# Kernel optimization log

Hardware: AMD Instinct MI355X
Metric: run time of the kernel (lower is better)

Reference implementation:

```python
import jax, jax.numpy as jnp
import numpy as np

D_MODEL = 1024

def setup_inputs() -> dict:
    key = jax.random.key(0)
    ks = jax.random.split(key, 5)
    s = 1.0 / np.sqrt(D_MODEL)  # torch Linear default init scale-ish
    x = jax.random.normal(ks[0], (4, 2048, D_MODEL), dtype=jnp.float32)
    Wq = jax.random.normal(ks[1], (D_MODEL, D_MODEL), dtype=jnp.float32) * s
    Wk = jax.random.normal(ks[2], (D_MODEL, D_MODEL), dtype=jnp.float32) * s
    Wv = jax.random.normal(ks[3], (D_MODEL, D_MODEL), dtype=jnp.float32) * s
    Wo = jax.random.normal(ks[4], (D_MODEL, D_MODEL), dtype=jnp.float32) * s
    z = jnp.zeros((D_MODEL,), dtype=jnp.float32)
    return {"x": x, "Wq": Wq, "bq": z, "Wk": Wk, "bk": z, "Wv": Wv, "bv": z, "Wo": Wo, "bo": z}

def reference(x, Wq, bq, Wk, bk, Wv, bv, Wo, bo):
    # x: (B, S, D). Single-head causal attention, dropout in eval mode (identity).
    B, S, D = x.shape
    Q = jnp.einsum('bsd,ed->bse', x, Wq) + bq
    K = jnp.einsum('bsd,ed->bse', x, Wk) + bk
    V = jnp.einsum('bsd,ed->bse', x, Wv) + bv
    scores = jnp.einsum('bqd,bkd->bqk', Q, K) / jnp.sqrt(jnp.float32(D))
    causal = jnp.tril(jnp.ones((S, S), dtype=bool))  # (S, S)
    scores = jnp.where(causal, scores, -jnp.inf)
    weights = jax.nn.softmax(scores, axis=-1)
    attended = jnp.einsum('bqk,bkd->bqd', weights, V)
    out = jnp.einsum('bsd,ed->bse', attended, Wo) + bo
    return out
```

## Files before the change

kernel.cpp:

```cpp
#include <hip/hip_runtime.h>
#include <cstdint>
#include <cstddef>


#define D_MODEL 1024
#define SEQ     2048
#define BATCH   4

typedef unsigned short u16;
typedef __bf16 bf16_t;
typedef bf16_t bf16x8 __attribute__((ext_vector_type(8)));
typedef float  f32x4  __attribute__((ext_vector_type(4)));
typedef u16    u16x4  __attribute__((ext_vector_type(4)));

__device__ __forceinline__ u16 f2bf(float x) {
  union { float f; uint32_t u; } v; v.f = x;
  uint32_t r = v.u + 0x7fffu + ((v.u >> 16) & 1u);
  return (u16)(r >> 16);
}

__device__ __forceinline__ void gload_lds16(const u16* g, u16* l) {
  __builtin_amdgcn_global_load_lds((__attribute__((address_space(1))) void*)g,
                                   (__attribute__((address_space(3))) void*)l,
                                   16, 0, 0);
}

template <bool ROWSUM>
__device__ __forceinline__ void gemm_core(const u16* __restrict__ Ablk,
                                          const u16* __restrict__ Bblk,
                                          int lda, int ldb, int ksteps64,
                                          u16* As, u16* Bs,
                                          f32x4 acc[4][4], f32x4* rs) {
  const int tid  = threadIdx.x;
  const int wave = tid >> 6, lane = tid & 63;
  const int wr = (wave >> 1) * 64, wc = (wave & 1) * 64;
  const int frow = lane & 15, kq = lane >> 4;
  int sm[4], sk[4];
#pragma unroll
  for (int t = 0; t < 4; ++t) {
    const int ch = t * 256 + tid;
    sm[t] = ch >> 3;
    sk[t] = ((ch & 7) ^ (sm[t] & 7)) * 8;
  }
  int aoff[4], boff[4];
#pragma unroll
  for (int i = 0; i < 4; ++i) {
    const int ra = wr + i * 16 + frow;
    aoff[i] = ra * 64 + ((kq ^ (ra & 7)) * 8);
    const int rb = wc + i * 16 + frow;
    boff[i] = rb * 64 + ((kq ^ (rb & 7)) * 8);
  }
  bf16x8 ones;
  if (ROWSUM) {
#pragma unroll
    for (int r = 0; r < 8; ++r) ((u16*)&ones)[r] = 0x3F80;
  }

  for (int kt = 0; kt < ksteps64; ++kt) {
    __syncthreads();
    const int kb = kt * 64;
#pragma unroll
    for (int t = 0; t < 4; ++t)
      gload_lds16(Ablk + sm[t] * lda + kb + sk[t], As + (t * 256 + tid) * 8);
#pragma unroll
    for (int t = 0; t < 4; ++t)
      gload_lds16(Bblk + sm[t] * ldb + kb + sk[t], Bs + (t * 256 + tid) * 8);
    asm volatile("s_waitcnt vmcnt(0)" ::: "memory");
    __syncthreads();

#pragma unroll
    for (int kh = 0; kh < 2; ++kh) {
      const int xo = kh * 32;
      bf16x8 af[4], bf[4];
#pragma unroll
      for (int i = 0; i < 4; ++i) af[i] = *(const bf16x8*)(As + (aoff[i] ^ xo));
#pragma unroll
      for (int j = 0; j < 4; ++j) bf[j] = *(const bf16x8*)(Bs + (boff[j] ^ xo));
#pragma unroll
      for (int i = 0; i < 4; ++i)
#pragma unroll
        for (int j = 0; j < 4; ++j)
          acc[i][j] = __builtin_amdgcn_mfma_f32_16x16x32_bf16(af[i], bf[j], acc[i][j], 0, 0, 0);
      if (ROWSUM) {
#pragma unroll
        for (int i = 0; i < 4; ++i)
          rs[i] = __builtin_amdgcn_mfma_f32_16x16x32_bf16(af[i], ones, rs[i], 0, 0, 0);
      }
    }
  }
}

__global__ __launch_bounds__(256) void cvt_kernel(const float4* __restrict__ x,
                                                  const float4* __restrict__ wq,
                                                  const float4* __restrict__ wk,
                                                  const float4* __restrict__ wv,
                                                  const float4* __restrict__ wo,
                                                  u16* __restrict__ dst) {
  const int i = blockIdx.x * 256 + threadIdx.x;
  float4 v;
  if (i < 2097152) {
    v = x[i];
  } else {
    const int j = i - 2097152;
    const int w = j >> 18;
    const float4* s = (w == 0) ? wq : (w == 1) ? wk : (w == 2) ? wv : wo;
    v = s[j & 262143];
  }
  u16x4 o = {f2bf(v.x), f2bf(v.y), f2bf(v.z), f2bf(v.w)};
  *(u16x4*)(dst + (size_t)i * 4) = o;
}

__global__ void transposeW_kernel(const u16* __restrict__ src, u16* __restrict__ dst) {
  __shared__ u16 tile[32][33];
  const int r0 = blockIdx.x * 32, c0 = blockIdx.y * 32;
  const int tx = threadIdx.x, ty = threadIdx.y;
#pragma unroll
  for (int r = 0; r < 4; ++r)
    tile[ty + r * 8][tx] = src[(size_t)(r0 + ty + r * 8) * D_MODEL + c0 + tx];
  __syncthreads();
#pragma unroll
  for (int r = 0; r < 4; ++r)
    dst[(size_t)(c0 + ty + r * 8) * D_MODEL + r0 + tx] = tile[tx][ty + r * 8];
}

__global__ __launch_bounds__(256) void stageA_kernel(
    const u16* __restrict__ xb,
    const u16* __restrict__ WqB, const u16* __restrict__ WkB,
    const u16* __restrict__ WoB, const u16* __restrict__ WvT,
    const float* __restrict__ Wo32, const float* __restrict__ bv,
    const float* __restrict__ bq, const float* __restrict__ bk,
    u16* __restrict__ Qb, u16* __restrict__ Kb,
    u16* __restrict__ Wp, float* __restrict__ bp) {
  __shared__ __align__(16) u16 As[128 * 64];
  __shared__ __align__(16) u16 Bs[128 * 64];
  const int blk = blockIdx.x;
  const int lane = threadIdx.x & 63, wave = threadIdx.x >> 6;
  const int wr = (wave >> 1) * 64, wc = (wave & 1) * 64;
  const int cl = lane & 15, rl = (lane >> 4) * 4;

  if (blk < 64) {
    const int f0 = (blk >> 3) * 128, e0 = (blk & 7) * 128;
    f32x4 acc[4][4] = {};
    gemm_core<false>(WoB + (size_t)f0 * D_MODEL, WvT + (size_t)e0 * D_MODEL,
                     D_MODEL, D_MODEL, 16, As, Bs, acc, nullptr);
#pragma unroll
    for (int j = 0; j < 4; ++j) {
      const int col = e0 + wc + j * 16 + cl;
#pragma unroll
      for (int i = 0; i < 4; ++i)
#pragma unroll
        for (int r = 0; r < 4; ++r) {
          const int row = f0 + wr + i * 16 + rl + r;
          Wp[(size_t)row * D_MODEL + col] = f2bf(acc[i][j][r]);
        }
    }
  } else if (blk < 80) {
    const int f = (blk - 64) * 64 + (threadIdx.x >> 2);
    const int dq = threadIdx.x & 3;
    const float* row = Wo32 + (size_t)f * D_MODEL + dq * 256;
    const float* bvq = bv + dq * 256;
    float s = 0.f;
#pragma unroll 8
    for (int i = 0; i < 256; ++i) s += row[i] * bvq[i];
    s += __shfl_xor(s, 1);
    s += __shfl_xor(s, 2);
    if (dq == 0) bp[f] = s;
  } else {
    const int v = blk - 80;
    const int c = v & 7, s = v >> 3;
    const int row0 = (c * 8 + (s >> 4)) * 128;
    const int cz = s & 15;
    const int z = cz >> 3;
    const int col0 = (cz & 7) * 128;
    const u16*   W    = z ? WkB : WqB;
    const float* bias = z ? bk : bq;
    u16*         out  = z ? Kb : Qb;
    f32x4 acc[4][4] = {};
    gemm_core<false>(xb + (size_t)row0 * D_MODEL, W + (size_t)col0 * D_MODEL,
                     D_MODEL, D_MODEL, 16, As, Bs, acc, nullptr);
#pragma unroll
    for (int j = 0; j < 4; ++j) {
      const int col = col0 + wc + j * 16 + cl;
      const float bb = bias[col];
#pragma unroll
      for (int i = 0; i < 4; ++i)
#pragma unroll
        for (int r = 0; r < 4; ++r) {
          const int row = row0 + wr + i * 16 + rl + r;
          out[(size_t)row * D_MODEL + col] = f2bf(acc[i][j][r] + bb);
        }
    }
  }
}

__global__ __launch_bounds__(256) void stageB_kernel(
    const u16* __restrict__ xb, const u16* __restrict__ Wp,
    const float* __restrict__ bp,
    const u16* __restrict__ Qb, const u16* __restrict__ Kb,
    u16* __restrict__ Vt, u16* __restrict__ Eb) {
  __shared__ __align__(16) u16 As[128 * 64];
  __shared__ __align__(16) u16 Bs[128 * 64];
  const int blk = blockIdx.x;
  const int lane = threadIdx.x & 63, wave = threadIdx.x >> 6;
  const int wr = (wave >> 1) * 64, wc = (wave & 1) * 64;
  const int cl = lane & 15, rl = (lane >> 4) * 4;

  if (blk < 544) {
    const int c = blk & 7, s = blk >> 3;
    int b, qi, ji;
    if (s < 48) {
      static const int sq_tab[6] = {1, 2, 2, 3, 3, 3};
      static const int sj_tab[6] = {0, 0, 1, 0, 1, 2};
      const int fi = c * 3 + (s >> 4);
      const int off = s & 15;
      b = fi / 6;
      const int fs = fi % 6;
      qi = sq_tab[fs] * 4 + (off >> 2);
      ji = sj_tab[fs] * 4 + (off & 3);
    } else {
      static const int di_tab[10] = {0, 1, 1, 2, 2, 2, 3, 3, 3, 3};
      static const int dj_tab[10] = {0, 0, 1, 0, 1, 2, 0, 1, 2, 3};
      const int k = (s - 48) / 10;
      const int off = (s - 48) % 10;
      const int di = c * 2 + k;
      b = di >> 2;
      const int dk = di & 3;
      qi = dk * 4 + di_tab[off];
      ji = dk * 4 + dj_tab[off];
    }
    const u16* A  = Qb + (size_t)(b * SEQ + qi * 128) * D_MODEL;
    const u16* Bt = Kb + (size_t)(b * SEQ + ji * 128) * D_MODEL;
    f32x4 acc[4][4] = {};
    gemm_core<false>(A, Bt, D_MODEL, D_MODEL, 16, As, Bs, acc, nullptr);
    u16* out = Eb + (size_t)b * SEQ * SEQ;
#pragma unroll
    for (int i = 0; i < 4; ++i)
#pragma unroll
      for (int r = 0; r < 4; ++r) {
        const int q = qi * 128 + wr + i * 16 + rl + r;
#pragma unroll
        for (int j = 0; j < 4; ++j) {
          const int jj = ji * 128 + wc + j * 16 + cl;
          out[(size_t)q * SEQ + jj] =
              (jj <= q) ? f2bf(__expf(acc[i][j][r] * 0.03125f)) : (u16)0;
        }
      }
  } else {
    const int v = blk - 544;
    const int c = v & 7, s = v >> 3;
    const int row0 = (c * 8 + (s >> 3)) * 128;
    const int col0 = (s & 7) * 128;
    f32x4 acc[4][4] = {};
    gemm_core<false>(xb + (size_t)row0 * D_MODEL, Wp + (size_t)col0 * D_MODEL,
                     D_MODEL, D_MODEL, 16, As, Bs, acc, nullptr);
    const int b = row0 >> 11;
    u16* vt = Vt + (size_t)b * D_MODEL * SEQ;
#pragma unroll
    for (int j = 0; j < 4; ++j) {
      const int col = col0 + wc + j * 16 + cl;
      const float bb = bp[col];
#pragma unroll
      for (int i = 0; i < 4; ++i) {
        const int s0 = (row0 & 2047) + wr + i * 16 + rl;
        u16x4 o = {f2bf(acc[i][j][0] + bb), f2bf(acc[i][j][1] + bb),
                   f2bf(acc[i][j][2] + bb), f2bf(acc[i][j][3] + bb)};
        *(u16x4*)(vt + (size_t)col * SEQ + s0) = o;
      }
    }
  }
}

__global__ __launch_bounds__(256) void pv_kernel(const u16* __restrict__ Eb,
                                                 const u16* __restrict__ Vt,
                                                 const float* __restrict__ bo,
                                                 float* __restrict__ Out) {
  __shared__ __align__(16) u16 As[128 * 64];
  __shared__ __align__(16) u16 Bs[128 * 64];
  const int u = blockIdx.x;
  const int c = u & 7, s = u >> 3;
  const int b  = c >> 1;
  const int dt = (c & 1) * 4 + (s >> 4);
  const int qt = 15 - (s & 15);
  const u16* A  = Eb + (size_t)b * SEQ * SEQ + (size_t)(qt * 128) * SEQ;
  const u16* Bt = Vt + (size_t)b * D_MODEL * SEQ + (size_t)(dt * 128) * SEQ;
  f32x4 acc[4][4] = {};
  f32x4 rs[4] = {};
  gemm_core<true>(A, Bt, SEQ, SEQ, (qt + 1) * 2, As, Bs, acc, rs);
  const int lane = threadIdx.x & 63, wave = threadIdx.x >> 6;
  const int wr = (wave >> 1) * 64, wc = (wave & 1) * 64;
  const int cl = lane & 15, rl = (lane >> 4) * 4;
#pragma unroll
  for (int i = 0; i < 4; ++i)
#pragma unroll
    for (int r = 0; r < 4; ++r) {
      const float invl = 1.0f / rs[i][r];
      const int row = b * SEQ + qt * 128 + wr + i * 16 + rl + r;
#pragma unroll
      for (int j = 0; j < 4; ++j) {
        const int col = dt * 128 + wc + j * 16 + cl;
        Out[(size_t)row * D_MODEL + col] = acc[i][j][r] * invl + bo[col];
      }
    }
}

extern "C" void kernel_launch(void* const* d_in, const int* in_sizes, int n_in,
                              void* d_out, int out_size, void* d_ws, size_t ws_size,
                              hipStream_t stream) {
  const float* x  = (const float*)d_in[0];
  const float* Wq = (const float*)d_in[1];
  const float* bq = (const float*)d_in[2];
  const float* Wk = (const float*)d_in[3];
  const float* bk = (const float*)d_in[4];
  const float* Wv = (const float*)d_in[5];
  const float* bv = (const float*)d_in[6];
  const float* Wo = (const float*)d_in[7];
  const float* bo = (const float*)d_in[8];
  float* out = (float*)d_out;
  char* ws = (char*)d_ws;

  u16*   xb  = (u16*)(ws);
  u16*   Wb  = (u16*)(ws + (16u << 20));
  u16*   Qb  = (u16*)(ws + (24u << 20));
  u16*   Kb  = (u16*)(ws + (40u << 20));
  u16*   Vt  = (u16*)(ws + (56u << 20));
  u16*   Eb  = (u16*)(ws + (72u << 20));
  u16*   WvT = (u16*)(ws + (104u << 20));
  u16*   Wp  = (u16*)(ws + (106u << 20));
  float* bp  = (float*)(ws + (108u << 20));

  cvt_kernel<<<12288, 256, 0, stream>>>((const float4*)x, (const float4*)Wq,
                                        (const float4*)Wk, (const float4*)Wv,
                                        (const float4*)Wo, xb);
  transposeW_kernel<<<dim3(32, 32), dim3(32, 8), 0, stream>>>(Wb + (2u << 20), WvT);
  stageA_kernel<<<1104, 256, 0, stream>>>(xb, Wb, Wb + (1u << 20), Wb + (3u << 20),
                                          WvT, Wo, bv, bq, bk, Qb, Kb, Wp, bp);
  stageB_kernel<<<1056, 256, 0, stream>>>(xb, Wp, bp, Qb, Kb, Vt, Eb);
  pv_kernel<<<512, 256, 0, stream>>>(Eb, Vt, bo, out);
}
```

Measured before the change: 268.2 us.

## Double-buffer GEMM core with 32-wide K tiles and prefetch overlap

Replaces the single-buffered 64-wide K-step loop with a double-buffered 32-wide K loop. The next tile's global-to-LDS loads are issued before computing on the current buffer, and a partial vmcnt wait lets the loads overlap the MFMAs. LDS use per block stays the same, and the XOR swizzle is re-derived for 4 chunks per row. The risk is twice as many iterations with two barriers each, plus a redundant final prefetch of the last tile.

```diff
diff --git a/kernel.cpp b/kernel.cpp
--- a/kernel.cpp
+++ b/kernel.cpp
@@ -28,27 +28,23 @@
 template <bool ROWSUM>
 __device__ __forceinline__ void gemm_core(const u16* __restrict__ Ablk,
                                           const u16* __restrict__ Bblk,
-                                          int lda, int ldb, int ksteps64,
+                                          int lda, int ldb, int ksteps32,
                                           u16* As, u16* Bs,
                                           f32x4 acc[4][4], f32x4* rs) {
   const int tid  = threadIdx.x;
   const int wave = tid >> 6, lane = tid & 63;
   const int wr = (wave >> 1) * 64, wc = (wave & 1) * 64;
-  const int frow = lane & 15, kq = lane >> 4;
-  int sm[4], sk[4];
-#pragma unroll
-  for (int t = 0; t < 4; ++t) {
-    const int ch = t * 256 + tid;
-    sm[t] = ch >> 3;
-    sk[t] = ((ch & 7) ^ (sm[t] & 7)) * 8;
-  }
+  const int frow = lane & 15, kc = lane >> 4;
+  const int ch0 = tid, ch1 = 256 + tid;
+  const int m0 = ch0 >> 2, k80 = (((ch0 & 3) ^ ((m0 >> 1) & 3))) * 8;
+  const int m1 = ch1 >> 2, k81 = (((ch1 & 3) ^ ((m1 >> 1) & 3))) * 8;
   int aoff[4], boff[4];
 #pragma unroll
   for (int i = 0; i < 4; ++i) {
     const int ra = wr + i * 16 + frow;
-    aoff[i] = ra * 64 + ((kq ^ (ra & 7)) * 8);
+    aoff[i] = (ra * 4 + (kc ^ ((ra >> 1) & 3))) * 8;
     const int rb = wc + i * 16 + frow;
-    boff[i] = rb * 64 + ((kq ^ (rb & 7)) * 8);
+    boff[i] = (rb * 4 + (kc ^ ((rb >> 1) & 3))) * 8;
   }
   bf16x8 ones;
   if (ROWSUM) {
@@ -56,37 +52,38 @@
     for (int r = 0; r < 8; ++r) ((u16*)&ones)[r] = 0x3F80;
   }
 
-  for (int kt = 0; kt < ksteps64; ++kt) {
-    __syncthreads();
-    const int kb = kt * 64;
-#pragma unroll
-    for (int t = 0; t < 4; ++t)
-      gload_lds16(Ablk + sm[t] * lda + kb + sk[t], As + (t * 256 + tid) * 8);
-#pragma unroll
-    for (int t = 0; t < 4; ++t)
-      gload_lds16(Bblk + sm[t] * ldb + kb + sk[t], Bs + (t * 256 + tid) * 8);
-    asm volatile("s_waitcnt vmcnt(0)" ::: "memory");
-    __syncthreads();
-
-#pragma unroll
-    for (int kh = 0; kh < 2; ++kh) {
-      const int xo = kh * 32;
-      bf16x8 af[4], bf[4];
-#pragma unroll
-      for (int i = 0; i < 4; ++i) af[i] = *(const bf16x8*)(As + (aoff[i] ^ xo));
-#pragma unroll
-      for (int j = 0; j < 4; ++j) bf[j] = *(const bf16x8*)(Bs + (boff[j] ^ xo));
+  gload_lds16(Ablk + m0 * lda + k80, As + ch0 * 8);
+  gload_lds16(Ablk + m1 * lda + k81, As + ch1 * 8);
+  gload_lds16(Bblk + m0 * ldb + k80, Bs + ch0 * 8);
+  gload_lds16(Bblk + m1 * ldb + k81, Bs + ch1 * 8);
+
+  for (int kt = 0; kt < ksteps32; ++kt) {
+    const int cur = (kt & 1) << 12;
+    const int nxt = cur ^ 4096;
+    const int kb = (kt + 1 < ksteps32 ? kt + 1 : kt) * 32;
+    gload_lds16(Ablk + m0 * lda + kb + k80, As + nxt + ch0 * 8);
+    gload_lds16(Ablk + m1 * lda + kb + k81, As + nxt + ch1 * 8);
+    gload_lds16(Bblk + m0 * ldb + kb + k80, Bs + nxt + ch0 * 8);
+    gload_lds16(Bblk + m1 * ldb + kb + k81, Bs + nxt + ch1 * 8);
+    asm volatile("s_waitcnt vmcnt(4)" ::: "memory");
+    asm volatile("s_barrier" ::: "memory");
+
+    bf16x8 af[4], bf[4];
+#pragma unroll
+    for (int i = 0; i < 4; ++i) af[i] = *(const bf16x8*)(As + cur + aoff[i]);
+#pragma unroll
+    for (int j = 0; j < 4; ++j) bf[j] = *(const bf16x8*)(Bs + cur + boff[j]);
+#pragma unroll
+    for (int i = 0; i < 4; ++i)
+#pragma unroll
+      for (int j = 0; j < 4; ++j)
+        acc[i][j] = __builtin_amdgcn_mfma_f32_16x16x32_bf16(af[i], bf[j], acc[i][j], 0, 0, 0);
+    if (ROWSUM) {
 #pragma unroll
       for (int i = 0; i < 4; ++i)
-#pragma unroll
-        for (int j = 0; j < 4; ++j)
-          acc[i][j] = __builtin_amdgcn_mfma_f32_16x16x32_bf16(af[i], bf[j], acc[i][j], 0, 0, 0);
-      if (ROWSUM) {
-#pragma unroll
-        for (int i = 0; i < 4; ++i)
-          rs[i] = __builtin_amdgcn_mfma_f32_16x16x32_bf16(af[i], ones, rs[i], 0, 0, 0);
-      }
-    }
+        rs[i] = __builtin_amdgcn_mfma_f32_16x16x32_bf16(af[i], ones, rs[i], 0, 0, 0);
+    }
+    asm volatile("s_barrier" ::: "memory");
   }
 }
 
@@ -131,8 +128,8 @@
     const float* __restrict__ bq, const float* __restrict__ bk,
     u16* __restrict__ Qb, u16* __restrict__ Kb,
     u16* __restrict__ Wp, float* __restrict__ bp) {
-  __shared__ __align__(16) u16 As[128 * 64];
-  __shared__ __align__(16) u16 Bs[128 * 64];
+  __shared__ __align__(16) u16 As[2 * 4096];
+  __shared__ __align__(16) u16 Bs[2 * 4096];
   const int blk = blockIdx.x;
   const int lane = threadIdx.x & 63, wave = threadIdx.x >> 6;
   const int wr = (wave >> 1) * 64, wc = (wave & 1) * 64;
@@ -142,7 +139,7 @@
     const int f0 = (blk >> 3) * 128, e0 = (blk & 7) * 128;
     f32x4 acc[4][4] = {};
     gemm_core<false>(WoB + (size_t)f0 * D_MODEL, WvT + (size_t)e0 * D_MODEL,
-                     D_MODEL, D_MODEL, 16, As, Bs, acc, nullptr);
+                     D_MODEL, D_MODEL, 32, As, Bs, acc, nullptr);
 #pragma unroll
     for (int j = 0; j < 4; ++j) {
       const int col = e0 + wc + j * 16 + cl;
@@ -177,7 +174,7 @@
     u16*         out  = z ? Kb : Qb;
     f32x4 acc[4][4] = {};
     gemm_core<false>(xb + (size_t)row0 * D_MODEL, W + (size_t)col0 * D_MODEL,
-                     D_MODEL, D_MODEL, 16, As, Bs, acc, nullptr);
+                     D_MODEL, D_MODEL, 32, As, Bs, acc, nullptr);
 #pragma unroll
     for (int j = 0; j < 4; ++j) {
       const int col = col0 + wc + j * 16 + cl;
@@ -198,8 +195,8 @@
     const float* __restrict__ bp,
     const u16* __restrict__ Qb, const u16* __restrict__ Kb,
     u16* __restrict__ Vt, u16* __restrict__ Eb) {
-  __shared__ __align__(16) u16 As[128 * 64];
-  __shared__ __align__(16) u16 Bs[128 * 64];
+  __shared__ __align__(16) u16 As[2 * 4096];
+  __shared__ __align__(16) u16 Bs[2 * 4096];
   const int blk = blockIdx.x;
   const int lane = threadIdx.x & 63, wave = threadIdx.x >> 6;
   const int wr = (wave >> 1) * 64, wc = (wave & 1) * 64;
@@ -231,7 +228,7 @@
     const u16* A  = Qb + (size_t)(b * SEQ + qi * 128) * D_MODEL;
     const u16* Bt = Kb + (size_t)(b * SEQ + ji * 128) * D_MODEL;
     f32x4 acc[4][4] = {};
-    gemm_core<false>(A, Bt, D_MODEL, D_MODEL, 16, As, Bs, acc, nullptr);
+    gemm_core<false>(A, Bt, D_MODEL, D_MODEL, 32, As, Bs, acc, nullptr);
     u16* out = Eb + (size_t)b * SEQ * SEQ;
 #pragma unroll
     for (int i = 0; i < 4; ++i)
@@ -252,7 +249,7 @@
     const int col0 = (s & 7) * 128;
     f32x4 acc[4][4] = {};
     gemm_core<false>(xb + (size_t)row0 * D_MODEL, Wp + (size_t)col0 * D_MODEL,
-                     D_MODEL, D_MODEL, 16, As, Bs, acc, nullptr);
+                     D_MODEL, D_MODEL, 32, As, Bs, acc, nullptr);
     const int b = row0 >> 11;
     u16* vt = Vt + (size_t)b * D_MODEL * SEQ;
 #pragma unroll
@@ -274,8 +271,8 @@
                                                  const u16* __restrict__ Vt,
                                                  const float* __restrict__ bo,
                                                  float* __restrict__ Out) {
-  __shared__ __align__(16) u16 As[128 * 64];
-  __shared__ __align__(16) u16 Bs[128 * 64];
+  __shared__ __align__(16) u16 As[2 * 4096];
+  __shared__ __align__(16) u16 Bs[2 * 4096];
   const int u = blockIdx.x;
   const int c = u & 7, s = u >> 3;
   const int b  = c >> 1;
@@ -285,7 +282,7 @@
   const u16* Bt = Vt + (size_t)b * D_MODEL * SEQ + (size_t)(dt * 128) * SEQ;
   f32x4 acc[4][4] = {};
   f32x4 rs[4] = {};
-  gemm_core<true>(A, Bt, SEQ, SEQ, (qt + 1) * 2, As, Bs, acc, rs);
+  gemm_core<true>(A, Bt, SEQ, SEQ, (qt + 1) * 4, As, Bs, acc, rs);
   const int lane = threadIdx.x & 63, wave = threadIdx.x >> 6;
   const int wr = (wave >> 1) * 64, wc = (wave & 1) * 64;
   const int cl = lane & 15, rl = (lane >> 4) * 4;
```

New measurement: 273.0 us. Within noise of the previous version (+1.8%).
